# Optimization experiments

Hardware: AMD Instinct MI355X
Metric: run time of the kernel (lower is better)

Reference implementation:

```python
import jax, jax.numpy as jnp
import numpy as np

N_LAYER = 2


def setup_inputs() -> dict:
    key = jax.random.key(0)
    k1, k2 = jax.random.split(key)
    seq_len, batch, hidden = 2048, 32, 512
    x = jax.random.normal(k1, (seq_len, batch, hidden), dtype=jnp.float32)
    # torch init: uniform(0, 1) on recurrent weights
    w_hh = jax.random.uniform(k2, (N_LAYER, hidden), dtype=jnp.float32)
    h0 = jnp.zeros((N_LAYER, batch, hidden), dtype=jnp.float32)
    return {"x": x, "w_hh": w_hh, "h0": h0}


def reference(x, w_hh, h0):
    # x: [T, B, H]; w_hh: [L, H]; h0: [L, B, H]
    out = x
    for i in range(N_LAYER):
        w = w_hh[i]  # [H]

        def step(h, xt):
            h_new = jax.nn.relu(xt + h * w)
            return h_new, h_new

        _, out = jax.lax.scan(step, h0[i], out)  # out: [T, B, H]
    return out
```

## Files before the change

kernel.cpp:

```cpp
#include <hip/hip_runtime.h>


#define TSTEPS  2048
#define BATCH   32
#define HID     512
#define BH      (BATCH * HID)
#define PHASE_T 64
#define NPHASE  (TSTEPS / PHASE_T)
#define NSLOT   4
#define SLOT_FLOATS (PHASE_T * 64)
#define SLOT_BYTES  (SLOT_FLOATS * 4)
#define LOADS_PER_PHASE (PHASE_T / 4)

typedef __attribute__((address_space(1))) const void* gas_cvp;
typedef __attribute__((address_space(3))) void*       las_vp;

__global__ __launch_bounds__(128, 1) void indrnn_pc_kernel(
    const float* __restrict__ x,
    const float* __restrict__ w_hh,
    const float* __restrict__ h0,
    float* __restrict__ out) {
  __shared__ float lds[NSLOT * SLOT_FLOATS];

  const int tid   = threadIdx.x;
  const int wave  = tid >> 6;
  const int lane  = tid & 63;
  const int cbase = blockIdx.x * 64;

  if (wave == 0) {
    const int j = lane >> 4;
    const int i = lane & 15;
    const float* gp = x + cbase + (size_t)j * BH + i * 4;

#pragma unroll
    for (int p = 0; p < 3; ++p) {
      char* lbase = (char*)lds + p * SLOT_BYTES;
      const float* gq = gp + (size_t)p * PHASE_T * BH;
#pragma unroll
      for (int q = 0; q < LOADS_PER_PHASE; ++q) {
        __builtin_amdgcn_global_load_lds((gas_cvp)(gq + (size_t)q * 4 * BH),
                                         (las_vp)(lbase + q * 1024), 16, 0, 0);
      }
    }
    __builtin_amdgcn_sched_barrier(0);
    asm volatile("s_waitcnt vmcnt(32)" ::: "memory");
    __builtin_amdgcn_s_barrier();

    for (int p = 0; p < NPHASE; ++p) {
      const int ip = p + 3;
      if (ip < NPHASE) {
        char* lbase = (char*)lds + (ip & (NSLOT - 1)) * SLOT_BYTES;
        const float* gq = gp + (size_t)ip * PHASE_T * BH;
#pragma unroll
        for (int q = 0; q < LOADS_PER_PHASE; ++q) {
          __builtin_amdgcn_global_load_lds((gas_cvp)(gq + (size_t)q * 4 * BH),
                                           (las_vp)(lbase + q * 1024), 16, 0, 0);
        }
      }
      __builtin_amdgcn_sched_barrier(0);
      if (p < NPHASE - 3)       asm volatile("s_waitcnt vmcnt(32)" ::: "memory");
      else if (p == NPHASE - 3) asm volatile("s_waitcnt vmcnt(16)" ::: "memory");
      else                      asm volatile("s_waitcnt vmcnt(0)"  ::: "memory");
      __builtin_amdgcn_s_barrier();
    }
  } else {
    const int c   = cbase + lane;
    const int hid = c & (HID - 1);
    const float w1 = w_hh[hid];
    const float w2 = w_hh[HID + hid];
    float h1 = h0[c];
    float h2 = h0[BH + c];
    float* op = out + c;

    for (int p = 0; p < NPHASE; ++p) {
      __builtin_amdgcn_s_barrier();
      __builtin_amdgcn_sched_barrier(0);
      const float* lb = lds + (p & (NSLOT - 1)) * SLOT_FLOATS + lane;
      float* ob = op + (size_t)p * PHASE_T * BH;
#pragma unroll
      for (int u = 0; u < PHASE_T; ++u) {
        const float xv = lb[u * 64];
        h1 = fmaxf(fmaf(w1, h1, xv), 0.0f);
        h2 = fmaxf(fmaf(w2, h2, h1), 0.0f);
        ob[(size_t)u * BH] = h2;
      }
      __builtin_amdgcn_sched_barrier(0);
    }
    __builtin_amdgcn_s_barrier();
  }
}

extern "C" void kernel_launch(void* const* d_in, const int* in_sizes, int n_in,
                              void* d_out, int out_size, void* d_ws, size_t ws_size,
                              hipStream_t stream) {
  const float* x    = (const float*)d_in[0];
  const float* w_hh = (const float*)d_in[1];
  const float* h0   = (const float*)d_in[2];
  float* out        = (float*)d_out;

  dim3 grid(BH / 64);
  dim3 block(128);
  hipLaunchKernelGGL(indrnn_pc_kernel, grid, block, 0, stream,
                     x, w_hh, h0, out);
}
```

Before: 231.0 us.

## Spread async x prefetch across four producer waves with deeper slot ring

Replaces the single producer wave with four producer waves. Each owns every fourth phase and issues global-to-LDS loads for it, so more loads are in flight per block. Phase length is halved and the ring grows to eight slots, keeping roughly eight phases of prefetch ahead of the consumer wave. This is meant to hide more of the global load latency on the serial recurrence, at the cost of a larger block and tighter barrier coordination between waves.

```diff
diff --git a/kernel.cpp b/kernel.cpp
--- a/kernel.cpp
+++ b/kernel.cpp
@@ -5,17 +5,29 @@
 #define BATCH   32
 #define HID     512
 #define BH      (BATCH * HID)
-#define PHASE_T 64
+#define PHASE_T 32
 #define NPHASE  (TSTEPS / PHASE_T)
-#define NSLOT   4
+#define NSLOT   8
 #define SLOT_FLOATS (PHASE_T * 64)
 #define SLOT_BYTES  (SLOT_FLOATS * 4)
-#define LOADS_PER_PHASE (PHASE_T / 4)
+#define LPP     (PHASE_T / 4)
+#define NPROD   4
 
 typedef __attribute__((address_space(1))) const void* gas_cvp;
 typedef __attribute__((address_space(3))) void*       las_vp;
 
-__global__ __launch_bounds__(128, 1) void indrnn_pc_kernel(
+#define ISSUE(q)                                                              \
+  do {                                                                        \
+    char* lb_ = (char*)lds + ((q) & (NSLOT - 1)) * SLOT_BYTES;                \
+    const float* gq_ = gp + (size_t)(q) * PHASE_T * BH;                       \
+    _Pragma("unroll")                                                         \
+    for (int m_ = 0; m_ < LPP; ++m_) {                                        \
+      __builtin_amdgcn_global_load_lds((gas_cvp)(gq_ + (size_t)m_ * 4 * BH),  \
+                                       (las_vp)(lb_ + m_ * 1024), 16, 0, 0);  \
+    }                                                                         \
+  } while (0)
+
+__global__ __launch_bounds__(320, 1) void indrnn_mp_kernel(
     const float* __restrict__ x,
     const float* __restrict__ w_hh,
     const float* __restrict__ h0,
@@ -27,41 +39,25 @@
   const int lane  = tid & 63;
   const int cbase = blockIdx.x * 64;
 
-  if (wave == 0) {
+  if (wave < NPROD) {
+    const int k = wave;
     const int j = lane >> 4;
     const int i = lane & 15;
     const float* gp = x + cbase + (size_t)j * BH + i * 4;
 
-#pragma unroll
-    for (int p = 0; p < 3; ++p) {
-      char* lbase = (char*)lds + p * SLOT_BYTES;
-      const float* gq = gp + (size_t)p * PHASE_T * BH;
-#pragma unroll
-      for (int q = 0; q < LOADS_PER_PHASE; ++q) {
-        __builtin_amdgcn_global_load_lds((gas_cvp)(gq + (size_t)q * 4 * BH),
-                                         (las_vp)(lbase + q * 1024), 16, 0, 0);
-      }
-    }
-    __builtin_amdgcn_sched_barrier(0);
-    asm volatile("s_waitcnt vmcnt(32)" ::: "memory");
-    __builtin_amdgcn_s_barrier();
+    ISSUE(k);
+    ISSUE(k + 4);
 
     for (int p = 0; p < NPHASE; ++p) {
-      const int ip = p + 3;
-      if (ip < NPHASE) {
-        char* lbase = (char*)lds + (ip & (NSLOT - 1)) * SLOT_BYTES;
-        const float* gq = gp + (size_t)ip * PHASE_T * BH;
-#pragma unroll
-        for (int q = 0; q < LOADS_PER_PHASE; ++q) {
-          __builtin_amdgcn_global_load_lds((gas_cvp)(gq + (size_t)q * 4 * BH),
-                                           (las_vp)(lbase + q * 1024), 16, 0, 0);
-        }
+      if ((p & 3) == k) {
+        __builtin_amdgcn_sched_barrier(0);
+        if (p + 4 < NPHASE) asm volatile("s_waitcnt vmcnt(8)" ::: "memory");
+        else                asm volatile("s_waitcnt vmcnt(0)" ::: "memory");
       }
+      __builtin_amdgcn_s_barrier();
       __builtin_amdgcn_sched_barrier(0);
-      if (p < NPHASE - 3)       asm volatile("s_waitcnt vmcnt(32)" ::: "memory");
-      else if (p == NPHASE - 3) asm volatile("s_waitcnt vmcnt(16)" ::: "memory");
-      else                      asm volatile("s_waitcnt vmcnt(0)"  ::: "memory");
-      __builtin_amdgcn_s_barrier();
+      const int q = p + 7;
+      if (q >= 8 && q < NPHASE && (q & 3) == k) ISSUE(q);
     }
   } else {
     const int c   = cbase + lane;
@@ -86,7 +82,6 @@
       }
       __builtin_amdgcn_sched_barrier(0);
     }
-    __builtin_amdgcn_s_barrier();
   }
 }
 
@@ -99,7 +94,7 @@
   float* out        = (float*)d_out;
 
   dim3 grid(BH / 64);
-  dim3 block(128);
-  hipLaunchKernelGGL(indrnn_pc_kernel, grid, block, 0, stream,
+  dim3 block(320);
+  hipLaunchKernelGGL(indrnn_mp_kernel, grid, block, 0, stream,
                      x, w_hh, h0, out);
 }
```

Measured after the change: 234.1 us. No clear change (+1.3%).
